# Kernel tuning notes

Measured on AMD Instinct MI355X. Metric: run time of the kernel, lower is better.

## Reference

```python
import jax, jax.numpy as jnp
import numpy as np

N = 50000          # nodes
E = 800000         # edges (avg in-degree 16)
F = 128            # hidden_dim
AVG_LOG = float(np.log(17.0))  # PyG avg_deg['log'] from deg histogram concentrated at degree 16
BN_EPS = 1e-5
STD_EPS = 1e-5


def setup_inputs() -> dict:
    key = jax.random.key(0)
    ks = jax.random.split(key, 10)
    h = jax.random.normal(ks[0], (N, F), dtype=jnp.float32)
    edge_index = jax.random.randint(ks[1], (2, E), 0, N, dtype=jnp.int64)

    def lin_w(k, fan_in, fan_out):
        return jax.random.normal(k, (fan_in, fan_out), dtype=jnp.float32) / np.sqrt(fan_in)

    return {
        "h": h,
        "edge_index": edge_index,
        "W_pre": lin_w(ks[2], 2 * F, F),   # pre_nn: Linear(2F -> F) on [x_i, x_j]
        "b_pre": jnp.zeros((F,), jnp.float32),
        "W_post": lin_w(ks[3], 13 * F, F),  # post_nn: Linear((1 + 4*3)F -> F)
        "b_post": jnp.zeros((F,), jnp.float32),
        "W_lin": lin_w(ks[4], F, F),       # final Linear(F -> F)
        "b_lin": jnp.zeros((F,), jnp.float32),
        "gamma": jnp.ones((F,), jnp.float32),   # BatchNorm1d weight
        "beta": jnp.zeros((F,), jnp.float32),   # BatchNorm1d bias
    }


def reference(h, edge_index, W_pre, b_pre, W_post, b_post, W_lin, b_lin, gamma, beta):
    src = edge_index[0]  # x_j (message source)
    dst = edge_index[1]  # x_i (aggregation target)
    n = h.shape[0]

    # pre_nn on concat([x_i, x_j])  -> per-edge message [E, F]
    m = jnp.concatenate([h[dst], h[src]], axis=-1) @ W_pre + b_pre

    # multi-aggregator scatter: mean, min, max, std (PyG order)
    cnt = jax.ops.segment_sum(jnp.ones((m.shape[0],), m.dtype), dst, num_segments=n)  # [N]
    deg = jnp.maximum(cnt, 1.0)[:, None]                                              # clamp(1)
    mean = jax.ops.segment_sum(m, dst, num_segments=n) / deg
    mean_sq = jax.ops.segment_sum(m * m, dst, num_segments=n) / deg
    std = jnp.sqrt(jax.nn.relu(mean_sq - mean * mean) + STD_EPS)
    has = (cnt > 0)[:, None]
    mn = jnp.where(has, jax.ops.segment_min(m, dst, num_segments=n), 0.0)
    mx = jnp.where(has, jax.ops.segment_max(m, dst, num_segments=n), 0.0)
    aggr = jnp.concatenate([mean, mn, mx, std], axis=-1)  # [N, 4F]

    # degree scalers: identity, amplification, attenuation
    logd = jnp.log(deg + 1.0)
    out = jnp.concatenate(
        [aggr, aggr * (logd / AVG_LOG), aggr * (AVG_LOG / logd)], axis=-1
    )  # [N, 12F]

    # update: concat self features, post_nn, final lin
    out = jnp.concatenate([h, out], axis=-1) @ W_post + b_post  # [N, F]
    out = out @ W_lin + b_lin

    # BatchNorm1d (training-mode batch statistics, biased variance) + ReLU
    mu = out.mean(axis=0)
    var = out.var(axis=0)
    out = (out - mu) / jnp.sqrt(var + BN_EPS) * gamma + beta
    out = jax.nn.relu(out)
    # dropout p=0.0 is identity; residual add
    return out + h
```

## Files before the change

### kernel.cpp

```cpp
#include <hip/hip_runtime.h>
#include <hip/hip_bf16.h>
#include <cstdint>
#include <cstddef>

typedef short s16x8 __attribute__((ext_vector_type(8)));
typedef float f32x4 __attribute__((ext_vector_type(4)));

#define AVG_LOG_F 2.8332133f

static __device__ __forceinline__ float b2f(unsigned short u) {
  union { unsigned int i; float f; } x; x.i = ((unsigned int)u) << 16; return x.f;
}
static __device__ __forceinline__ unsigned short f2b(float f) {
  __hip_bfloat16 h = __float2bfloat16(f);
  union { __hip_bfloat16 hh; unsigned short u; } c; c.hh = h; return c.u;
}
static __device__ __forceinline__ unsigned int pack2(float lo, float hi) {
  return (unsigned int)f2b(lo) | ((unsigned int)f2b(hi) << 16);
}
static __device__ __forceinline__ int swz(int row, int slot) {
  return row * 32 + ((slot ^ ((row >> 1) & 3)) << 3);
}

__global__ void conv_h_kernel(const float* __restrict__ h, unsigned short* __restrict__ hb, int total4) {
  int i = blockIdx.x * blockDim.x + threadIdx.x;
  if (i >= total4) return;
  const float4 v = ((const float4*)h)[i];
  uint2 r;
  r.x = pack2(v.x, v.y);
  r.y = pack2(v.z, v.w);
  ((uint2*)hb)[i] = r;
}

__global__ void fold_wcat_kernel(const float* __restrict__ W_pre, unsigned short* __restrict__ WcatT) {
  int idx = blockIdx.x * blockDim.x + threadIdx.x;
  int c = idx >> 7, k = idx & 127;
  float v = (c < 128) ? W_pre[k * 128 + c] : W_pre[(128 + k) * 128 + (c - 128)];
  WcatT[c * 128 + k] = f2b(v);
}

__global__ __launch_bounds__(128) void fold_wpost_kernel(
    const float* __restrict__ W_post, const float* __restrict__ b_post,
    const float* __restrict__ W_lin, const float* __restrict__ b_lin,
    unsigned short* __restrict__ WfoldT, float* __restrict__ bfold) {
  __shared__ float wl[128 * 128];
  const int j = threadIdx.x;
  for (int r = 0; r < 128; ++r) wl[r * 128 + j] = W_lin[r * 128 + j];
  __syncthreads();
  if (blockIdx.x == 208) {
    float acc = b_lin[j];
    for (int k = 0; k < 128; ++k) acc += b_post[k] * wl[k * 128 + j];
    bfold[j] = acc;
  } else {
#pragma unroll 2
    for (int ii = 0; ii < 8; ++ii) {
      const int i = blockIdx.x * 8 + ii;
      float acc = 0.f;
      for (int k = 0; k < 128; ++k) acc += W_post[i * 128 + k] * wl[k * 128 + j];
      WfoldT[(size_t)j * 1664 + i] = f2b(acc);
    }
  }
}

__global__ void bucket_hist_kernel(const int* __restrict__ dst, int* __restrict__ bucketCnt, int E) {
  __shared__ int lcnt[256];
  const int tid = threadIdx.x;
  lcnt[tid] = 0;
  __syncthreads();
  for (int e = blockIdx.x * 256 + tid; e < E; e += gridDim.x * 256)
    atomicAdd(&lcnt[dst[e] >> 8], 1);
  __syncthreads();
  if (lcnt[tid] > 0) atomicAdd(&bucketCnt[tid], lcnt[tid]);
}

__global__ void bucket_scan_kernel(const int* __restrict__ bucketCnt, int* __restrict__ bucketBase,
                                   int* __restrict__ bucketCursor, int* __restrict__ rowptr,
                                   int n, int nb, int E) {
  __shared__ int sh[256];
  const int tid = threadIdx.x;
  const int v = (tid < nb) ? bucketCnt[tid] : 0;
  sh[tid] = v;
  __syncthreads();
  for (int o = 1; o < 256; o <<= 1) {
    int t = (tid >= o) ? sh[tid - o] : 0;
    __syncthreads();
    sh[tid] += t;
    __syncthreads();
  }
  const int base = sh[tid] - v;
  if (tid < nb) { bucketBase[tid] = base; bucketCursor[tid] = base; }
  if (tid == nb - 1) bucketBase[nb] = base + v;
  if (tid == 0) rowptr[n] = E;
}

__global__ __launch_bounds__(256) void s1_scatter_kernel(
    const int* __restrict__ src, const int* __restrict__ dst,
    int* __restrict__ bucketCursor, unsigned int* __restrict__ bucketed, int E, int CH) {
  __shared__ int lcnt[256], loff[256], lcur[256], gbase[256];
  __shared__ unsigned int stage[5000];
  __shared__ unsigned char sbid[5000];
  const int tid = threadIdx.x;
  const int c0 = blockIdx.x * CH;
  const int c1 = min(c0 + CH, E);
  const int cnt = c1 - c0;
  if (cnt <= 0) return;
  lcnt[tid] = 0;
  __syncthreads();
  for (int e = c0 + tid; e < c1; e += 256) atomicAdd(&lcnt[dst[e] >> 8], 1);
  __syncthreads();
  const int v = lcnt[tid];
  loff[tid] = 0;
  __syncthreads();
  {
    __shared__ int tmp[256];
    tmp[tid] = v;
    __syncthreads();
    for (int o = 1; o < 256; o <<= 1) {
      int t = (tid >= o) ? tmp[tid - o] : 0;
      __syncthreads();
      tmp[tid] += t;
      __syncthreads();
    }
    loff[tid] = tmp[tid] - v;
  }
  lcur[tid] = loff[tid];
  gbase[tid] = (v > 0) ? atomicAdd(&bucketCursor[tid], v) : 0;
  __syncthreads();
  for (int e = c0 + tid; e < c1; e += 256) {
    const int d = dst[e];
    const int b = d >> 8;
    const int slot = atomicAdd(&lcur[b], 1);
    stage[slot] = ((unsigned int)(d & 255) << 16) | (unsigned int)src[e];
    sbid[slot] = (unsigned char)b;
  }
  __syncthreads();
  for (int i = tid; i < cnt; i += 256) {
    const int b = sbid[i];
    bucketed[gbase[b] + (i - loff[b])] = stage[i];
  }
}

__global__ __launch_bounds__(256) void s2_build_kernel(
    const unsigned int* __restrict__ bucketed, const int* __restrict__ bucketBase,
    int* __restrict__ rowptr, unsigned short* __restrict__ ssrc, int n) {
  __shared__ int ncnt[256], noff[256], ncur[256];
  __shared__ unsigned short csr16[8192];
  const int tid = threadIdx.x;
  const int b = blockIdx.x;
  const int seg0 = bucketBase[b], seg1 = bucketBase[b + 1];
  const int cnt = seg1 - seg0;
  ncnt[tid] = 0;
  __syncthreads();
  for (int i = tid; i < cnt; i += 256) atomicAdd(&ncnt[bucketed[seg0 + i] >> 16], 1);
  __syncthreads();
  const int v = ncnt[tid];
  {
    __shared__ int tmp[256];
    tmp[tid] = v;
    __syncthreads();
    for (int o = 1; o < 256; o <<= 1) {
      int t = (tid >= o) ? tmp[tid - o] : 0;
      __syncthreads();
      tmp[tid] += t;
      __syncthreads();
    }
    noff[tid] = tmp[tid] - v;
  }
  ncur[tid] = noff[tid];
  const int node = (b << 8) + tid;
  if (node < n) rowptr[node] = seg0 + noff[tid];
  __syncthreads();
  for (int i = tid; i < cnt; i += 256) {
    const unsigned int rec = bucketed[seg0 + i];
    const int d = rec >> 16;
    const int slot = atomicAdd(&ncur[d], 1);
    if (slot < 8192) csr16[slot] = (unsigned short)(rec & 0xffffu);
  }
  __syncthreads();
  for (int i = tid; i < cnt; i += 256) ssrc[seg0 + i] = csr16[i];
}

__global__ __launch_bounds__(256) void gemm256_kernel(
    const unsigned short* __restrict__ A, const unsigned short* __restrict__ BT,
    unsigned short* __restrict__ outb, int M)
{
  constexpr int LDT = 40;
  constexpr int K = 128, NK = K / 32;
  __shared__ alignas(16) unsigned short Asm[2][128 * LDT];
  __shared__ alignas(16) unsigned short Bsm[2][128 * LDT];
  const int tid = threadIdx.x, lane = tid & 63;
  const int w = tid >> 6, wr = w >> 1, wc = w & 1;
  const int row0 = blockIdx.x * 128;
  const int col0 = blockIdx.y * 128;
  const int srow = tid >> 2, slot = tid & 3;
  const int ar0 = min(row0 + srow, M - 1);
  const int ar1 = min(row0 + srow + 64, M - 1);
  const unsigned short* ap0 = A + (size_t)ar0 * K + slot * 8;
  const unsigned short* ap1 = A + (size_t)ar1 * K + slot * 8;
  const unsigned short* bp0 = BT + (size_t)(col0 + srow) * K + slot * 8;
  const unsigned short* bp1 = BT + (size_t)(col0 + srow + 64) * K + slot * 8;
  const int wa0 = srow * LDT + slot * 8, wa1 = wa0 + 64 * LDT;

  int offA[4], offB[4];
#pragma unroll
  for (int i = 0; i < 4; ++i) {
    offA[i] = (wr * 64 + i * 16 + (lane & 15)) * LDT + (lane >> 4) * 8;
    offB[i] = (wc * 64 + i * 16 + (lane & 15)) * LDT + (lane >> 4) * 8;
  }

  f32x4 acc[4][4] = {};
  uint4 a0 = *(const uint4*)ap0;
  uint4 a1 = *(const uint4*)ap1;
  uint4 b0 = *(const uint4*)bp0;
  uint4 b1 = *(const uint4*)bp1;
  *(uint4*)&Asm[0][wa0] = a0; *(uint4*)&Asm[0][wa1] = a1;
  *(uint4*)&Bsm[0][wa0] = b0; *(uint4*)&Bsm[0][wa1] = b1;
  __syncthreads();

  for (int kt = 0; kt < NK; ++kt) {
    const int cur = kt & 1;
    if (kt + 1 < NK) {
      const int k0 = (kt + 1) * 32;
      a0 = *(const uint4*)(ap0 + k0); a1 = *(const uint4*)(ap1 + k0);
      b0 = *(const uint4*)(bp0 + k0); b1 = *(const uint4*)(bp1 + k0);
    }
    s16x8 af[4], bq[4];
#pragma unroll
    for (int i = 0; i < 4; ++i) af[i] = *(const s16x8*)&Asm[cur][offA[i]];
#pragma unroll
    for (int i = 0; i < 4; ++i) bq[i] = *(const s16x8*)&Bsm[cur][offB[i]];
#pragma unroll
    for (int mi = 0; mi < 4; ++mi)
#pragma unroll
      for (int ni = 0; ni < 4; ++ni)
        acc[mi][ni] = __builtin_amdgcn_mfma_f32_16x16x32_bf16(af[mi], bq[ni], acc[mi][ni], 0, 0, 0);
    if (kt + 1 < NK) {
      const int nxt = cur ^ 1;
      *(uint4*)&Asm[nxt][wa0] = a0; *(uint4*)&Asm[nxt][wa1] = a1;
      *(uint4*)&Bsm[nxt][wa0] = b0; *(uint4*)&Bsm[nxt][wa1] = b1;
      __syncthreads();
    }
  }

#pragma unroll
  for (int mi = 0; mi < 4; ++mi) {
#pragma unroll
    for (int ni = 0; ni < 4; ++ni) {
      const int rbase = row0 + wr * 64 + mi * 16 + (lane >> 4) * 4;
      const int c = col0 + wc * 64 + ni * 16 + (lane & 15);
#pragma unroll
      for (int r = 0; r < 4; ++r) {
        const int rr = rbase + r;
        if (rr < M) outb[(size_t)rr * 256 + c] = f2b(acc[mi][ni][r]);
      }
    }
  }
}

#define AGG_EDGE(IDX)                                                                  \
  {                                                                                    \
    const unsigned int v = *(const unsigned int*)(AB + (size_t)(IDX) * 256 + 128 + 2 * lane); \
    const float v0 = b2f((unsigned short)(v & 0xffffu));                               \
    const float v1 = b2f((unsigned short)(v >> 16));                                   \
    s0 += v0; q0 += v0 * v0; mn0 = fminf(mn0, v0); mx0 = fmaxf(mx0, v0);               \
    s1v += v1; q1 += v1 * v1; mn1 = fminf(mn1, v1); mx1 = fmaxf(mx1, v1);              \
  }

__global__ void aggregate_kernel(const unsigned short* __restrict__ AB,
                                 const unsigned short* __restrict__ hb,
                                 const float* __restrict__ b_pre,
                                 const int* __restrict__ rowptr, const unsigned short* __restrict__ ssrc,
                                 unsigned short* __restrict__ Xagg,
                                 float* __restrict__ sc1, float* __restrict__ sc2, int n) {
  const int node = blockIdx.x * 4 + (threadIdx.x >> 6);
  if (node >= n) return;
  const int lane = threadIdx.x & 63;
  const int beg = rowptr[node], end = rowptr[node + 1];
  const int cnt = end - beg;
  float s0 = 0.f, s1v = 0.f, q0 = 0.f, q1 = 0.f;
  float mn0 = 3.4e38f, mn1 = 3.4e38f, mx0 = -3.4e38f, mx1 = -3.4e38f;
  for (int base = beg; base < end; base += 64) {
    const int m = min(64, end - base);
    const int myidx = (base + lane < end) ? (int)ssrc[base + lane] : 0;
    int t = 0;
    for (; t + 8 <= m; t += 8) {
      const int i0 = __builtin_amdgcn_readlane(myidx, t + 0);
      const int i1 = __builtin_amdgcn_readlane(myidx, t + 1);
      const int i2 = __builtin_amdgcn_readlane(myidx, t + 2);
      const int i3 = __builtin_amdgcn_readlane(myidx, t + 3);
      const int i4 = __builtin_amdgcn_readlane(myidx, t + 4);
      const int i5 = __builtin_amdgcn_readlane(myidx, t + 5);
      const int i6 = __builtin_amdgcn_readlane(myidx, t + 6);
      const int i7 = __builtin_amdgcn_readlane(myidx, t + 7);
      AGG_EDGE(i0) AGG_EDGE(i1) AGG_EDGE(i2) AGG_EDGE(i3)
      AGG_EDGE(i4) AGG_EDGE(i5) AGG_EDGE(i6) AGG_EDGE(i7)
    }
    for (; t < m; ++t) {
      const int i0 = __builtin_amdgcn_readlane(myidx, t);
      AGG_EDGE(i0)
    }
  }
  const float degf = (float)(cnt > 0 ? cnt : 1);
  const float2 bp = ((const float2*)b_pre)[lane];
  const unsigned int cpair = *(const unsigned int*)(AB + (size_t)node * 256 + 2 * lane);
  const float c0 = b2f((unsigned short)(cpair & 0xffffu)) + bp.x;
  const float c1 = b2f((unsigned short)(cpair >> 16)) + bp.y;
  float mean0, mean1, std0, std1, lo0, lo1, hi0, hi1;
  if (cnt > 0) {
    const float inv = 1.f / degf;
    const float mu0 = s0 * inv, mu1 = s1v * inv;
    mean0 = c0 + mu0; mean1 = c1 + mu1;
    std0 = sqrtf(fmaxf(q0 * inv - mu0 * mu0, 0.f) + 1e-5f);
    std1 = sqrtf(fmaxf(q1 * inv - mu1 * mu1, 0.f) + 1e-5f);
    lo0 = c0 + mn0; lo1 = c1 + mn1; hi0 = c0 + mx0; hi1 = c1 + mx1;
  } else {
    mean0 = mean1 = lo0 = lo1 = hi0 = hi1 = 0.f;
    std0 = std1 = sqrtf(1e-5f);
  }
  const float logd = logf(degf + 1.f);
  unsigned int* row = (unsigned int*)(Xagg + (size_t)node * 640);
  row[lane]       = *(const unsigned int*)(hb + (size_t)node * 128 + 2 * lane);
  row[64 + lane]  = pack2(mean0, mean1);
  row[128 + lane] = pack2(lo0, lo1);
  row[192 + lane] = pack2(hi0, hi1);
  row[256 + lane] = pack2(std0, std1);
  if (lane == 0) { sc1[node] = logd / AVG_LOG_F; sc2[node] = AVG_LOG_F / logd; }
}

__global__ __launch_bounds__(512) void gemm_split_kernel(
    const unsigned short* __restrict__ Xagg, const float* __restrict__ sc1,
    const float* __restrict__ sc2, const unsigned short* __restrict__ WT,
    const float* __restrict__ bias, float* __restrict__ out3,
    float* __restrict__ bnsum, int M)
{
  constexpr int NK = 20;
  __shared__ alignas(16) unsigned short Asm[2][128 * 32];
  __shared__ alignas(16) unsigned short B0s[2][128 * 32];
  __shared__ alignas(16) unsigned short B1s[2][128 * 32];
  __shared__ alignas(16) unsigned short B2s[2][128 * 32];
  __shared__ float sLDS[2][128];
  __shared__ float bnacc[256];
  const int tid = threadIdx.x, lane = tid & 63, w = tid >> 6;
  const int wr = w >> 2, wc = w & 3;
  const int row0 = blockIdx.x * 128;
  const int srow = tid >> 2, slot = tid & 3;
  const int arow = min(row0 + srow, M - 1);
  const unsigned short* ap = Xagg + (size_t)arow * 640 + slot * 8;
  const unsigned short* bp = WT + (size_t)srow * 1664 + slot * 8;
  const int wa = swz(srow, slot);

  if (tid < 128) {
    const int rr = min(row0 + tid, M - 1);
    sLDS[0][tid] = sc1[rr];
    sLDS[1][tid] = sc2[rr];
  }
  if (tid < 256) bnacc[tid] = 0.f;

  int offA[4], offB[2];
#pragma unroll
  for (int i = 0; i < 4; ++i) offA[i] = swz(wr * 64 + i * 16 + (lane & 15), lane >> 4);
#pragma unroll
  for (int i = 0; i < 2; ++i) offB[i] = swz(wc * 32 + i * 16 + (lane & 15), lane >> 4);

  f32x4 acc0[4][2] = {}, acc1[4][2] = {}, acc2[4][2] = {};
  uint4 a = *(const uint4*)ap;
  uint4 b0 = *(const uint4*)bp;
  uint4 b1, b2;
  *(uint4*)&Asm[0][wa] = a;
  *(uint4*)&B0s[0][wa] = b0;
  __syncthreads();

  for (int kt = 0; kt < NK; ++kt) {
    const int cur = kt & 1;
    const bool pf = kt + 1 < NK;
    if (pf) {
      const int ka = (kt + 1) * 32;
      a = *(const uint4*)(ap + ka);
      b0 = *(const uint4*)(bp + ka);
      if (kt + 1 >= 4) {
        const int kb = ka - 128;
        b1 = *(const uint4*)(bp + 640 + kb);
        b2 = *(const uint4*)(bp + 1152 + kb);
      }
    }
    s16x8 af[4], q0[2];
#pragma unroll
    for (int i = 0; i < 4; ++i) af[i] = *(const s16x8*)&Asm[cur][offA[i]];
#pragma unroll
    for (int i = 0; i < 2; ++i) q0[i] = *(const s16x8*)&B0s[cur][offB[i]];
#pragma unroll
    for (int mi = 0; mi < 4; ++mi)
#pragma unroll
      for (int ni = 0; ni < 2; ++ni)
        acc0[mi][ni] = __builtin_amdgcn_mfma_f32_16x16x32_bf16(af[mi], q0[ni], acc0[mi][ni], 0, 0, 0);
    if (kt >= 4) {
      s16x8 q1[2], q2[2];
#pragma unroll
      for (int i = 0; i < 2; ++i) q1[i] = *(const s16x8*)&B1s[cur][offB[i]];
#pragma unroll
      for (int i = 0; i < 2; ++i) q2[i] = *(const s16x8*)&B2s[cur][offB[i]];
#pragma unroll
      for (int mi = 0; mi < 4; ++mi)
#pragma unroll
        for (int ni = 0; ni < 2; ++ni) {
          acc1[mi][ni] = __builtin_amdgcn_mfma_f32_16x16x32_bf16(af[mi], q1[ni], acc1[mi][ni], 0, 0, 0);
          acc2[mi][ni] = __builtin_amdgcn_mfma_f32_16x16x32_bf16(af[mi], q2[ni], acc2[mi][ni], 0, 0, 0);
        }
    }
    if (pf) {
      const int nxt = cur ^ 1;
      *(uint4*)&Asm[nxt][wa] = a;
      *(uint4*)&B0s[nxt][wa] = b0;
      if (kt + 1 >= 4) {
        *(uint4*)&B1s[nxt][wa] = b1;
        *(uint4*)&B2s[nxt][wa] = b2;
      }
      __syncthreads();
    }
  }

  float cs[2] = {0.f, 0.f}, css[2] = {0.f, 0.f};
#pragma unroll
  for (int mi = 0; mi < 4; ++mi) {
#pragma unroll
    for (int ni = 0; ni < 2; ++ni) {
      const int rbase = row0 + wr * 64 + mi * 16 + (lane >> 4) * 4;
      const int c = wc * 32 + ni * 16 + (lane & 15);
      const float bb = bias[c];
#pragma unroll
      for (int r = 0; r < 4; ++r) {
        const int rr = rbase + r;
        if (rr < M) {
          const int rl = rr - row0;
          const float v = acc0[mi][ni][r] + sLDS[0][rl] * acc1[mi][ni][r]
                        + sLDS[1][rl] * acc2[mi][ni][r] + bb;
          out3[(size_t)rr * 128 + c] = v;
          cs[ni] += v; css[ni] += v * v;
        }
      }
    }
  }
  __syncthreads();
#pragma unroll
  for (int ni = 0; ni < 2; ++ni) {
    const int c = wc * 32 + ni * 16 + (lane & 15);
    atomicAdd(&bnacc[c], cs[ni]);
    atomicAdd(&bnacc[128 + c], css[ni]);
  }
  __syncthreads();
  if (tid < 128) {
    atomicAdd(&bnsum[tid], bnacc[tid]);
    atomicAdd(&bnsum[128 + tid], bnacc[128 + tid]);
  }
}

__global__ void bnfinal_kernel(const float* __restrict__ bnsum, const float* __restrict__ gamma,
                               const float* __restrict__ beta, float* __restrict__ sc,
                               float* __restrict__ shv, int n) {
  const int f = threadIdx.x;
  const float inv = 1.f / (float)n;
  const float mu = bnsum[f] * inv;
  const float var = bnsum[128 + f] * inv - mu * mu;
  const float rstd = rsqrtf(var + 1e-5f);
  const float s = gamma[f] * rstd;
  sc[f] = s;
  shv[f] = beta[f] - mu * s;
}

__global__ void epilogue_kernel(const float* __restrict__ out3, const float* __restrict__ h,
                                const float* __restrict__ sc, const float* __restrict__ shv,
                                float* __restrict__ out, int total4) {
  int i = blockIdx.x * blockDim.x + threadIdx.x;
  if (i >= total4) return;
  const int c = (i & 31) * 4;
  const float4 x = ((const float4*)out3)[i];
  const float4 hh = ((const float4*)h)[i];
  float4 r;
  r.x = fmaxf(x.x * sc[c + 0] + shv[c + 0], 0.f) + hh.x;
  r.y = fmaxf(x.y * sc[c + 1] + shv[c + 1], 0.f) + hh.y;
  r.z = fmaxf(x.z * sc[c + 2] + shv[c + 2], 0.f) + hh.z;
  r.w = fmaxf(x.w * sc[c + 3] + shv[c + 3], 0.f) + hh.w;
  ((float4*)out)[i] = r;
}

extern "C" void kernel_launch(void* const* d_in, const int* in_sizes, int n_in,
                              void* d_out, int out_size, void* d_ws, size_t ws_size,
                              hipStream_t stream) {
  const float* h      = (const float*)d_in[0];
  const int*   ei     = (const int*)d_in[1];
  const float* W_pre  = (const float*)d_in[2];
  const float* b_pre  = (const float*)d_in[3];
  const float* W_post = (const float*)d_in[4];
  const float* b_post = (const float*)d_in[5];
  const float* W_lin  = (const float*)d_in[6];
  const float* b_lin  = (const float*)d_in[7];
  const float* gamma  = (const float*)d_in[8];
  const float* beta   = (const float*)d_in[9];

  const int n = in_sizes[0] / 128;
  const int E = in_sizes[1] / 2;
  const int* src = ei;
  const int* dst = ei + E;

  char* ws = (char*)d_ws;
  size_t off = 0;
  auto carve = [&](size_t bytes) {
    off = (off + 255) & ~(size_t)255;
    void* p = ws + off;
    off += bytes;
    return p;
  };
  unsigned short* hb   = (unsigned short*)carve((size_t)n * 128 * 2);
  void* ab_out3        = carve((size_t)n * 256 * 2);
  unsigned short* AB   = (unsigned short*)ab_out3;
  float* out3          = (float*)ab_out3;
  unsigned short* Xagg = (unsigned short*)carve((size_t)n * 640 * 2);
  float* sc1           = (float*)carve((size_t)n * 4);
  float* sc2           = (float*)carve((size_t)n * 4);
  unsigned short* WcatT  = (unsigned short*)carve(256 * 128 * 2);
  unsigned short* WfoldT = (unsigned short*)carve((size_t)128 * 1664 * 2);
  float* bfold         = (float*)carve(128 * 4);
  int*   bucketCnt     = (int*)carve(256 * 4);
  int*   bucketBase    = (int*)carve(257 * 4);
  int*   bucketCursor  = (int*)carve(256 * 4);
  unsigned int* bucketed = (unsigned int*)carve((size_t)E * 4);
  int*   rowptr        = (int*)carve((size_t)(n + 1) * 4);
  unsigned short* ssrc = (unsigned short*)carve((size_t)(E + 2) * 2);
  float* bnsum         = (float*)carve(256 * 4);
  float* bnsc          = (float*)carve(128 * 4);
  float* bnsh          = (float*)carve(128 * 4);

  const int total4 = n * 128 / 4;
  const int mt = (n + 127) / 128;
  const int nb = (n + 255) >> 8;
  const int nS1 = (E + 4999) / 5000;

  conv_h_kernel<<<(total4 + 255) / 256, 256, 0, stream>>>(h, hb, total4);
  fold_wcat_kernel<<<128, 256, 0, stream>>>(W_pre, WcatT);
  fold_wpost_kernel<<<209, 128, 0, stream>>>(W_post, b_post, W_lin, b_lin, WfoldT, bfold);

  hipMemsetAsync(bucketCnt, 0, 256 * 4, stream);
  hipMemsetAsync(bnsum, 0, 256 * 4, stream);
  bucket_hist_kernel<<<256, 256, 0, stream>>>(dst, bucketCnt, E);
  bucket_scan_kernel<<<1, 256, 0, stream>>>(bucketCnt, bucketBase, bucketCursor, rowptr, n, nb, E);
  s1_scatter_kernel<<<nS1, 256, 0, stream>>>(src, dst, bucketCursor, bucketed, E, 5000);
  s2_build_kernel<<<nb, 256, 0, stream>>>(bucketed, bucketBase, rowptr, ssrc, n);

  gemm256_kernel<<<dim3(mt, 2), 256, 0, stream>>>(hb, WcatT, AB, n);
  aggregate_kernel<<<(n + 3) / 4, 256, 0, stream>>>(AB, hb, b_pre, rowptr, ssrc, Xagg, sc1, sc2, n);
  gemm_split_kernel<<<mt, 512, 0, stream>>>(Xagg, sc1, sc2, WfoldT, bfold, out3, bnsum, n);

  bnfinal_kernel<<<1, 128, 0, stream>>>(bnsum, gamma, beta, bnsc, bnsh, n);
  epilogue_kernel<<<(total4 + 255) / 256, 256, 0, stream>>>(out3, h, bnsc, bnsh, (float*)d_out, total4);
}
```

Before: 291.9 us.

## Fold degree scalers into A operand to use single accumulator GEMM

Replaces the split GEMM, which kept three accumulators (identity, amplification, attenuation) and combined them with per-row scalers in the epilogue, with one K=1664 GEMM. The A tile is built on the fly by scaling the 512-wide aggregate slice with sc1 or sc2 per row before it is written to shared memory. This frees registers and shared memory (one B buffer instead of three) at the cost of re-reading the A rows three times and doing extra bf16 convert/multiply work per load. The pre-scaling is rounded to bf16, which slightly changes numerics.

Measured after the change: 299.1 us. 2.5% more time.

```diff
diff --git a/kernel.cpp b/kernel.cpp
--- a/kernel.cpp
+++ b/kernel.cpp
@@ -327,33 +327,42 @@
   if (lane == 0) { sc1[node] = logd / AVG_LOG_F; sc2[node] = AVG_LOG_F / logd; }
 }
 
-__global__ __launch_bounds__(512) void gemm_split_kernel(
+static __device__ __forceinline__ uint4 scale8(uint4 r, float s) {
+  union { uint4 v; unsigned short h[8]; } in, out;
+  in.v = r;
+#pragma unroll
+  for (int i = 0; i < 8; ++i) out.h[i] = f2b(b2f(in.h[i]) * s);
+  return out.v;
+}
+static __device__ __forceinline__ uint4 loadA_fold(const unsigned short* base, int kc,
+                                                   float s1v, float s2v) {
+  const bool m1 = kc >= 640;
+  const bool m2 = kc >= 1152;
+  const int off = kc - (m1 ? 512 : 0) - (m2 ? 512 : 0);
+  uint4 r = *(const uint4*)(base + off);
+  if (m1) r = scale8(r, m2 ? s2v : s1v);
+  return r;
+}
+
+__global__ __launch_bounds__(512) void gemm_fold2_kernel(
     const unsigned short* __restrict__ Xagg, const float* __restrict__ sc1,
     const float* __restrict__ sc2, const unsigned short* __restrict__ WT,
     const float* __restrict__ bias, float* __restrict__ out3,
     float* __restrict__ bnsum, int M)
 {
-  constexpr int NK = 20;
+  constexpr int NK = 52;
   __shared__ alignas(16) unsigned short Asm[2][128 * 32];
-  __shared__ alignas(16) unsigned short B0s[2][128 * 32];
-  __shared__ alignas(16) unsigned short B1s[2][128 * 32];
-  __shared__ alignas(16) unsigned short B2s[2][128 * 32];
-  __shared__ float sLDS[2][128];
+  __shared__ alignas(16) unsigned short Bsm[2][128 * 32];
   __shared__ float bnacc[256];
   const int tid = threadIdx.x, lane = tid & 63, w = tid >> 6;
   const int wr = w >> 2, wc = w & 3;
   const int row0 = blockIdx.x * 128;
   const int srow = tid >> 2, slot = tid & 3;
   const int arow = min(row0 + srow, M - 1);
-  const unsigned short* ap = Xagg + (size_t)arow * 640 + slot * 8;
-  const unsigned short* bp = WT + (size_t)srow * 1664 + slot * 8;
+  const unsigned short* abase = Xagg + (size_t)arow * 640;
+  const unsigned short* bbase = WT + (size_t)srow * 1664 + slot * 8;
+  const float s1v = sc1[arow], s2v = sc2[arow];
   const int wa = swz(srow, slot);
-
-  if (tid < 128) {
-    const int rr = min(row0 + tid, M - 1);
-    sLDS[0][tid] = sc1[rr];
-    sLDS[1][tid] = sc2[rr];
-  }
   if (tid < 256) bnacc[tid] = 0.f;
 
   int offA[4], offB[2];
@@ -362,59 +371,35 @@
 #pragma unroll
   for (int i = 0; i < 2; ++i) offB[i] = swz(wc * 32 + i * 16 + (lane & 15), lane >> 4);
 
-  f32x4 acc0[4][2] = {}, acc1[4][2] = {}, acc2[4][2] = {};
-  uint4 a = *(const uint4*)ap;
-  uint4 b0 = *(const uint4*)bp;
-  uint4 b1, b2;
+  f32x4 acc[4][2] = {};
+  uint4 a = loadA_fold(abase, slot * 8, s1v, s2v);
+  uint4 b = *(const uint4*)bbase;
   *(uint4*)&Asm[0][wa] = a;
-  *(uint4*)&B0s[0][wa] = b0;
+  *(uint4*)&Bsm[0][wa] = b;
   __syncthreads();
 
   for (int kt = 0; kt < NK; ++kt) {
     const int cur = kt & 1;
     const bool pf = kt + 1 < NK;
     if (pf) {
-      const int ka = (kt + 1) * 32;
-      a = *(const uint4*)(ap + ka);
-      b0 = *(const uint4*)(bp + ka);
-      if (kt + 1 >= 4) {
-        const int kb = ka - 128;
-        b1 = *(const uint4*)(bp + 640 + kb);
-        b2 = *(const uint4*)(bp + 1152 + kb);
-      }
-    }
-    s16x8 af[4], q0[2];
+      const int kc = (kt + 1) * 32 + slot * 8;
+      a = loadA_fold(abase, kc, s1v, s2v);
+      b = *(const uint4*)(bbase + (kt + 1) * 32);
+    }
+    s16x8 af[4], bq[2];
 #pragma unroll
     for (int i = 0; i < 4; ++i) af[i] = *(const s16x8*)&Asm[cur][offA[i]];
 #pragma unroll
-    for (int i = 0; i < 2; ++i) q0[i] = *(const s16x8*)&B0s[cur][offB[i]];
+    for (int i = 0; i < 2; ++i) bq[i] = *(const s16x8*)&Bsm[cur][offB[i]];
 #pragma unroll
     for (int mi = 0; mi < 4; ++mi)
 #pragma unroll
       for (int ni = 0; ni < 2; ++ni)
-        acc0[mi][ni] = __builtin_amdgcn_mfma_f32_16x16x32_bf16(af[mi], q0[ni], acc0[mi][ni], 0, 0, 0);
-    if (kt >= 4) {
-      s16x8 q1[2], q2[2];
-#pragma unroll
-      for (int i = 0; i < 2; ++i) q1[i] = *(const s16x8*)&B1s[cur][offB[i]];
-#pragma unroll
-      for (int i = 0; i < 2; ++i) q2[i] = *(const s16x8*)&B2s[cur][offB[i]];
-#pragma unroll
-      for (int mi = 0; mi < 4; ++mi)
-#pragma unroll
-        for (int ni = 0; ni < 2; ++ni) {
-          acc1[mi][ni] = __builtin_amdgcn_mfma_f32_16x16x32_bf16(af[mi], q1[ni], acc1[mi][ni], 0, 0, 0);
-          acc2[mi][ni] = __builtin_amdgcn_mfma_f32_16x16x32_bf16(af[mi], q2[ni], acc2[mi][ni], 0, 0, 0);
-        }
-    }
+        acc[mi][ni] = __builtin_amdgcn_mfma_f32_16x16x32_bf16(af[mi], bq[ni], acc[mi][ni], 0, 0, 0);
     if (pf) {
       const int nxt = cur ^ 1;
       *(uint4*)&Asm[nxt][wa] = a;
-      *(uint4*)&B0s[nxt][wa] = b0;
-      if (kt + 1 >= 4) {
-        *(uint4*)&B1s[nxt][wa] = b1;
-        *(uint4*)&B2s[nxt][wa] = b2;
-      }
+      *(uint4*)&Bsm[nxt][wa] = b;
       __syncthreads();
     }
   }
@@ -431,9 +416,7 @@
       for (int r = 0; r < 4; ++r) {
         const int rr = rbase + r;
         if (rr < M) {
-          const int rl = rr - row0;
-          const float v = acc0[mi][ni][r] + sLDS[0][rl] * acc1[mi][ni][r]
-                        + sLDS[1][rl] * acc2[mi][ni][r] + bb;
+          const float v = acc[mi][ni][r] + bb;
           out3[(size_t)rr * 128 + c] = v;
           cs[ni] += v; css[ni] += v * v;
         }
@@ -548,7 +531,7 @@
 
   gemm256_kernel<<<dim3(mt, 2), 256, 0, stream>>>(hb, WcatT, AB, n);
   aggregate_kernel<<<(n + 3) / 4, 256, 0, stream>>>(AB, hb, b_pre, rowptr, ssrc, Xagg, sc1, sc2, n);
-  gemm_split_kernel<<<mt, 512, 0, stream>>>(Xagg, sc1, sc2, WfoldT, bfold, out3, bnsum, n);
+  gemm_fold2_kernel<<<mt, 512, 0, stream>>>(Xagg, sc1, sc2, WfoldT, bfold, out3, bnsum, n);
 
   bnfinal_kernel<<<1, 128, 0, stream>>>(bnsum, gamma, beta, bnsc, bnsh, n);
   epilogue_kernel<<<(total4 + 255) / 256, 256, 0, stream>>>(out3, h, bnsc, bnsh, (float*)d_out, total4);
```
